# Kernel tuning notes

Hardware: AMD Instinct MI355X
Metric: run time of the kernel (lower is better)

The kernel has to match this reference:

```python
import jax, jax.numpy as jnp
import numpy as np
import math

H = 32          # num heads
D_NOPE = 128
D_ROPE = 64
D_QK = D_NOPE + D_ROPE   # 192
D_V = 128
KV_LORA = 512
EPS = 1e-6
ROPE_THETA = 10000.0
FACTOR = 40.0
BETA_FAST, BETA_SLOW = 32.0, 1.0
ORIG_MAX_POS = 4096
MSCALE_ALL_DIM = 1.0


def _yarn_inv_freq():
    dim = D_ROPE
    pos_freqs = ROPE_THETA ** (np.arange(0, dim, 2, dtype=np.float64) / dim)
    inv_extra = 1.0 / pos_freqs
    inv_inter = 1.0 / (FACTOR * pos_freqs)

    def corr_dim(n_rot):
        return dim * math.log(ORIG_MAX_POS / (n_rot * 2 * math.pi)) / (2 * math.log(ROPE_THETA))
    low = max(math.floor(corr_dim(BETA_FAST)), 0)
    high = min(math.ceil(corr_dim(BETA_SLOW)), dim - 1)
    ramp = np.clip((np.arange(dim // 2, dtype=np.float64) - low) / max(high - low, 1e-3), 0, 1)
    inv_freq_mask = 1.0 - ramp  # extrapolation_factor = 1
    inv_freq = inv_inter * (1 - inv_freq_mask) + inv_extra * inv_freq_mask
    return jnp.asarray(inv_freq, dtype=jnp.float32)  # [D_ROPE//2]


def _apply_rope_gptj(x, cos, sin):
    # x: [T, n, D_ROPE]; cos/sin: [T, D_ROPE//2]; interleaved (is_neox_style=False)
    x2 = x.reshape(*x.shape[:-1], D_ROPE // 2, 2)
    x1, xo = x2[..., 0], x2[..., 1]
    c = cos[:, None, :]
    s = sin[:, None, :]
    r1 = x1 * c - xo * s
    r2 = xo * c + x1 * s
    return jnp.stack([r1, r2], axis=-1).reshape(x.shape)


def _rmsnorm(x, w):
    var = jnp.mean(x.astype(jnp.float32) ** 2, axis=-1, keepdims=True)
    return (x * jax.lax.rsqrt(var + EPS)) * w


def setup_inputs() -> dict:
    key = jax.random.key(0)
    ks = jax.random.split(key, 8)
    T, HID = 2048, 4096
    def w(k, shape, fan_in):
        return jax.random.normal(k, shape, dtype=jnp.float32) * (1.0 / math.sqrt(fan_in))
    return {
        "positions": jnp.arange(T, dtype=jnp.int32),
        "hidden_states": jax.random.normal(ks[0], (T, HID), dtype=jnp.float32),
        "Wqa": w(ks[1], (HID, 1536), HID),
        "q_a_ln": jnp.ones((1536,), dtype=jnp.float32),
        "Wqb": w(ks[2], (1536, H * D_QK), 1536),
        "Wkva": w(ks[3], (HID, KV_LORA + D_ROPE), HID),
        "kv_a_ln": jnp.ones((KV_LORA,), dtype=jnp.float32),
        "Wkvb": w(ks[4], (KV_LORA, H * (D_NOPE + D_V)), KV_LORA),
        "Wo": w(ks[5], (H * D_V, HID), H * D_V),
    }


def reference(positions, hidden_states, Wqa, q_a_ln, Wqb, Wkva, kv_a_ln, Wkvb, Wo):
    T = hidden_states.shape[0]
    # softmax scaling with yarn mscale correction
    mscale = 0.1 * MSCALE_ALL_DIM * math.log(FACTOR) + 1.0
    scaling = (D_QK ** -0.5) * mscale * mscale

    # --- low-rank Q path ---
    q = hidden_states @ Wqa                       # [T, 1536]
    q = _rmsnorm(q, q_a_ln)
    q = (q @ Wqb).reshape(T, H, D_QK)             # [T, H, 192]
    q_nope, q_pe = q[..., :D_NOPE], q[..., D_NOPE:]

    # --- low-rank latent KV path ---
    latent = hidden_states @ Wkva                 # [T, 576]
    kv_a = _rmsnorm(latent[:, :KV_LORA], kv_a_ln) # [T, 512]
    k_pe = latent[:, None, KV_LORA:]              # [T, 1, 64]
    kv = (kv_a @ Wkvb).reshape(T, H, D_NOPE + D_V)
    k_nope = kv[..., :D_NOPE]                     # [T, H, 128]
    v = kv[..., D_NOPE:]                          # [T, H, 128]

    # --- decoupled RoPE on rope slice only ---
    inv_freq = _yarn_inv_freq()
    freqs = positions.astype(jnp.float32)[:, None] * inv_freq[None, :]  # [T, 32]
    cos, sin = jnp.cos(freqs), jnp.sin(freqs)
    q_pe = _apply_rope_gptj(q_pe, cos, sin)       # [T, H, 64]
    k_pe = _apply_rope_gptj(k_pe, cos, sin)       # [T, 1, 64]

    q = jnp.concatenate([q_nope, q_pe], axis=-1)                      # [T, H, 192]
    k = jnp.concatenate([k_nope, jnp.broadcast_to(k_pe, (T, H, D_ROPE))], axis=-1)

    # --- causal MHA over assembled K/V ---
    scores = jnp.einsum('thd,shd->hts', q, k) * scaling               # [H, T, T]
    causal = positions[None, :, None] >= positions[None, None, :]
    scores = jnp.where(causal, scores, jnp.finfo(scores.dtype).min)
    probs = jax.nn.softmax(scores, axis=-1)
    attn = jnp.einsum('hts,shd->thd', probs, v).reshape(T, H * D_V)
    return attn @ Wo                                                   # [T, 4096]
```

## Files before the change

kernel.cpp:

```cpp
#include <hip/hip_runtime.h>
#include <math.h>

typedef __bf16 bf16x8 __attribute__((ext_vector_type(8)));
typedef float f32x4 __attribute__((ext_vector_type(4)));
typedef unsigned short u16;
typedef unsigned int u32;

#define T_SEQ 2048
#define NHEAD 32

__device__ __forceinline__ u16 f2bu(float f){
  u32 u = __float_as_uint(f);
  u32 r = (u + 0x7fffu + ((u >> 16) & 1u)) >> 16;
  return (u16)r;
}

__device__ __forceinline__ void gload_lds16(const void* g, void* l){
  __builtin_amdgcn_global_load_lds((const __attribute__((address_space(1))) u32*)g,
                                   (__attribute__((address_space(3))) u32*)l, 16, 0, 0);
}

__global__ void cast_f32_bf16(const float* __restrict__ in, u16* __restrict__ out, int n4){
  int i = blockIdx.x * blockDim.x + threadIdx.x;
  int stride = gridDim.x * blockDim.x;
  for (; i < n4; i += stride){
    float4 v = ((const float4*)in)[i];
    ushort4 o;
    o.x = f2bu(v.x); o.y = f2bu(v.y); o.z = f2bu(v.z); o.w = f2bu(v.w);
    ((ushort4*)out)[i] = o;
  }
}

__global__ void transpose_cast(const float* __restrict__ src, u16* __restrict__ dst,
                               int K, int N){
  __shared__ float tile[64][65];
  int k0 = blockIdx.x * 64, n0 = blockIdx.y * 64;
  int lr = threadIdx.x >> 6, lc = threadIdx.x & 63;
  #pragma unroll
  for (int i = 0; i < 16; i++){
    int r = lr * 16 + i;
    int n = n0 + lc;
    float v = (n < N) ? src[(size_t)(k0 + r) * N + n] : 0.f;
    tile[r][lc] = v;
  }
  __syncthreads();
  #pragma unroll
  for (int i = 0; i < 16; i++){
    int nr = lr * 16 + i;
    dst[(size_t)(n0 + nr) * K + k0 + lc] = f2bu(tile[lc][nr]);
  }
}

__global__ void rope_table(const int* __restrict__ positions, float* __restrict__ cosT,
                           float* __restrict__ sinT, float lo, float denom){
  int idx = blockIdx.x * blockDim.x + threadIdx.x;
  if (idx >= T_SEQ * 32) return;
  int t = idx >> 5, i = idx & 31;
  float pf = powf(10000.f, (float)i / 32.f);
  float inv_extra = 1.f / pf;
  float inv_inter = 1.f / (40.f * pf);
  float ramp = fminf(fmaxf(((float)i - lo) / denom, 0.f), 1.f);
  float invf = inv_inter * ramp + inv_extra * (1.f - ramp);
  float fr = (float)positions[t] * invf;
  cosT[idx] = cosf(fr);
  sinT[idx] = sinf(fr);
}

__global__ void rmsnorm_cast(const float* __restrict__ in, int istride, int n,
                             const float* __restrict__ w, u16* __restrict__ out, int ostride){
  int row = blockIdx.x;
  const float* x = in + (size_t)row * istride;
  float ss = 0.f;
  for (int c = threadIdx.x; c < n; c += blockDim.x){ float v = x[c]; ss += v * v; }
  #pragma unroll
  for (int off = 1; off < 64; off <<= 1) ss += __shfl_xor(ss, off);
  __shared__ float wsum[4];
  if ((threadIdx.x & 63) == 0) wsum[threadIdx.x >> 6] = ss;
  __syncthreads();
  float tot = wsum[0] + wsum[1] + wsum[2] + wsum[3];
  float scale = rsqrtf(tot / (float)n + 1e-6f);
  for (int c = threadIdx.x; c < n; c += blockDim.x)
    out[(size_t)row * ostride + c] = f2bu(x[c] * scale * w[c]);
}

__global__ void rope_kpe(const float* __restrict__ lat, int lstride, int loff,
                         const float* __restrict__ cosT,
                         const float* __restrict__ sinT, u16* __restrict__ kpe){
  int idx = blockIdx.x * blockDim.x + threadIdx.x;
  if (idx >= T_SEQ * 32) return;
  int t = idx >> 5, i = idx & 31;
  float x1 = lat[(size_t)t * lstride + loff + 2 * i];
  float x2 = lat[(size_t)t * lstride + loff + 2 * i + 1];
  float c = cosT[idx], s = sinT[idx];
  kpe[t * 64 + 2 * i]     = f2bu(x1 * c - x2 * s);
  kpe[t * 64 + 2 * i + 1] = f2bu(x2 * c + x1 * s);
}

__global__ void kpe_bcast(const u16* __restrict__ kpe, u16* __restrict__ Kp){
  int idx = blockIdx.x * blockDim.x + threadIdx.x;
  if (idx >= NHEAD * T_SEQ * 16) return;
  int h = idx >> 15;
  int rem = idx & 32767;
  int t = rem >> 4, j = rem & 15;
  ushort4 v = ((const ushort4*)(kpe + t * 64))[j];
  ((ushort4*)(Kp + (size_t)h * T_SEQ * 192 + (size_t)t * 192 + 128))[j] = v;
}

__global__ void build_vt(const u16* __restrict__ Vtmp, u16* __restrict__ Vt){
  __shared__ u16 tile[128][72];
  int t0 = blockIdx.x * 64;
  int h = blockIdx.y;
  #pragma unroll
  for (int i = 0; i < 32; i++){
    int lin = threadIdx.x + i * 256;
    int tt = lin >> 7, dd = lin & 127;
    tile[dd][tt] = Vtmp[(size_t)(t0 + tt) * 4096 + h * 128 + dd];
  }
  __syncthreads();
  #pragma unroll
  for (int i = 0; i < 32; i++){
    int lin = threadIdx.x + i * 256;
    int dd = lin >> 6, tt = lin & 63;
    Vt[(size_t)(h * 128 + dd) * T_SEQ + t0 + tt] = tile[dd][tt];
  }
}

template<int EPI>
__global__ __launch_bounds__(256) void gemm_bt(const u16* __restrict__ A, const u16* __restrict__ BT,
                                               float* __restrict__ C, u16* __restrict__ O1,
                                               u16* __restrict__ O2,
                                               const float* __restrict__ cosT,
                                               const float* __restrict__ sinT,
                                               float scaling, int M, int N, int K){
  __shared__ __align__(1024) char lds[32768];
  const int tid = threadIdx.x;
  const int wave = tid >> 6, lane = tid & 63;
  const int lg = lane >> 4, lm = lane & 15;

  int gx = gridDim.x;
  int nwg = gx * gridDim.y;
  int orig = blockIdx.y * gx + blockIdx.x;
  int qq = nwg >> 3, rr = nwg & 7, xc = orig & 7, rest = orig >> 3;
  int wg = (xc < rr ? xc * (qq + 1) : rr * (qq + 1) + (xc - rr) * qq) + rest;
  const int bn = (wg % gx) * 128, bm = (wg / gx) * 128;

  const int wr = (wave >> 1) * 64, wc = (wave & 1) * 64;
  f32x4 acc[4][4] = {};
  int srow[2], scol[2], soff[2];
  #pragma unroll
  for (int j = 0; j < 2; j++){
    int o = (wave * 2 + j) * 1024 + lane * 16;
    int row = o >> 6;
    int cg = ((o >> 4) & 3) ^ ((row >> 1) & 3);
    srow[j] = row; scol[j] = cg * 8; soff[j] = (wave * 2 + j) * 1024;
  }

  #pragma unroll
  for (int j = 0; j < 2; j++){
    gload_lds16(A  + (size_t)(bm + srow[j]) * K + scol[j], lds + soff[j]);
    gload_lds16(BT + (size_t)(bn + srow[j]) * K + scol[j], lds + 16384 + soff[j]);
  }

  int cur = 0;
  for (int k0 = 0; k0 < K; k0 += 32){
    if (k0 + 32 < K){
      char* dA = lds + (cur ^ 1) * 8192;
      char* dB = lds + 16384 + (cur ^ 1) * 8192;
      #pragma unroll
      for (int j = 0; j < 2; j++){
        gload_lds16(A  + (size_t)(bm + srow[j]) * K + k0 + 32 + scol[j], dA + soff[j]);
        gload_lds16(BT + (size_t)(bn + srow[j]) * K + k0 + 32 + scol[j], dB + soff[j]);
      }
      asm volatile("s_waitcnt vmcnt(4)" ::: "memory");
    } else {
      asm volatile("s_waitcnt vmcnt(0)" ::: "memory");
    }
    __builtin_amdgcn_sched_barrier(0);
    __builtin_amdgcn_s_barrier();

    const char* ldsA = lds + cur * 8192;
    const char* ldsB = lds + 16384 + cur * 8192;
    bf16x8 af[4], bfr[4];
    #pragma unroll
    for (int m = 0; m < 4; m++){
      int r = wr + m * 16 + lm;
      af[m] = *(const bf16x8*)(ldsA + r * 64 + ((lg ^ ((r >> 1) & 3)) << 4));
    }
    #pragma unroll
    for (int n = 0; n < 4; n++){
      int r = wc + n * 16 + lm;
      bfr[n] = *(const bf16x8*)(ldsB + r * 64 + ((lg ^ ((r >> 1) & 3)) << 4));
    }
    __builtin_amdgcn_s_setprio(1);
    #pragma unroll
    for (int m = 0; m < 4; m++)
      #pragma unroll
      for (int n = 0; n < 4; n++)
        acc[m][n] = __builtin_amdgcn_mfma_f32_16x16x32_bf16(af[m], bfr[n], acc[m][n], 0, 0, 0);
    __builtin_amdgcn_s_setprio(0);
    __builtin_amdgcn_s_barrier();
    cur ^= 1;
  }

  #pragma unroll
  for (int m = 0; m < 4; m++)
    #pragma unroll
    for (int n = 0; n < 4; n++)
      #pragma unroll
      for (int q = 0; q < 4; q++){
        int r = bm + wr + m * 16 + lg * 4 + q;
        int c = bn + wc + n * 16 + lm;
        float v = acc[m][n][q];
        if (EPI == 0){
          C[(size_t)r * N + c] = v;
        } else if (EPI == 1){
          float vp = __shfl_xor(v, 1);
          int h = c / 192, d = c - h * 192;
          float outv;
          if (d < 128) outv = v;
          else {
            int i = (d - 128) >> 1;
            float co = cosT[r * 32 + i], si = sinT[r * 32 + i];
            outv = (d & 1) ? (v * co + vp * si) : (v * co - vp * si);
          }
          O1[(size_t)h * T_SEQ * 192 + (size_t)r * 192 + d] = f2bu(outv * scaling);
        } else {
          int h = c >> 8, d = c & 255;
          if (d < 128) O1[(size_t)h * T_SEQ * 192 + (size_t)r * 192 + d] = f2bu(v);
          else         O2[(size_t)r * 4096 + h * 128 + (d - 128)] = f2bu(v);
        }
      }
}

__global__ __launch_bounds__(512, 1) void flash_attn(const u16* __restrict__ Qp, const u16* __restrict__ Kp,
                                                     const u16* __restrict__ Vt, u16* __restrict__ attnb){
  const int b = blockIdx.x;
  const int h = (b & 7) + 8 * ((b >> 3) & 3);
  const int s = b >> 5;
  const int tid = threadIdx.x;
  const int wave = tid >> 6, lane = tid & 63;
  const int lg = lane >> 4, lm = lane & 15;

  __shared__ __align__(1024) char lds[100352];
  char* ldsK = lds;
  char* ldsV = lds + 49152;
  u16*  Pw   = (u16*)(lds + 81920 + wave * 2304);

  const u16* KpH = Kp + (size_t)h * T_SEQ * 192;
  const u16* VtH = Vt + (size_t)h * 128 * T_SEQ;

  int kO[3], kSrc[3];
  #pragma unroll
  for (int j = 0; j < 3; j++){
    int o = (tid + 512 * j) * 16;
    int r = o / 384, c = (o % 384) >> 4;
    kO[j] = o; kSrc[j] = r * 192 + ((c ^ (r & 7)) << 3);
  }
  int vO[2], vSrc[2];
  #pragma unroll
  for (int j = 0; j < 2; j++){
    int o = (tid + 512 * j) * 16;
    int d = o >> 7, c = (o & 127) >> 4;
    vO[j] = o; vSrc[j] = d * T_SEQ + ((c ^ (d & 7)) << 3);
  }

  #pragma unroll 1
  for (int rep = 0; rep < 2; rep++){
    const int qt = rep ? s : (15 - s);
    const int qbase = qt * 128 + wave * 16;
    const int nt = 2 * qt + 2;

    __syncthreads();

    bf16x8 qf[6];
    const u16* Qbase = Qp + (size_t)(h * T_SEQ + qbase + lm) * 192 + lg * 8;
    #pragma unroll
    for (int dk = 0; dk < 6; dk++) qf[dk] = *(const bf16x8*)(Qbase + dk * 32);

    f32x4 o_[8] = {};
    float m_[4], l_[4];
    #pragma unroll
    for (int q = 0; q < 4; q++){ m_[q] = -3.0e38f; l_[q] = 0.f; }

    #pragma unroll
    for (int j = 0; j < 3; j++) gload_lds16(KpH + kSrc[j], ldsK + kO[j]);
    #pragma unroll
    for (int j = 0; j < 2; j++) gload_lds16(VtH + vSrc[j], ldsV + vO[j]);

    for (int kt = 0; kt < nt; kt++){
      const int t0 = kt * 64;
      const int bsel = kt & 1;
      asm volatile("s_waitcnt vmcnt(0)" ::: "memory");
      __builtin_amdgcn_sched_barrier(0);
      __builtin_amdgcn_s_barrier();
      if (kt + 1 < nt){
        const int t1 = t0 + 64;
        char* Kd = ldsK + (bsel ^ 1) * 24576;
        char* Vd = ldsV + (bsel ^ 1) * 16384;
        #pragma unroll
        for (int j = 0; j < 3; j++) gload_lds16(KpH + (size_t)t1 * 192 + kSrc[j], Kd + kO[j]);
        #pragma unroll
        for (int j = 0; j < 2; j++) gload_lds16(VtH + vSrc[j] + t1, Vd + vO[j]);
      }
      const char* Kb = ldsK + bsel * 24576;
      const char* Vb = ldsV + bsel * 16384;

      f32x4 s_[4] = {};
      __builtin_amdgcn_s_setprio(1);
      #pragma unroll
      for (int hh = 0; hh < 4; hh++){
        const int r = hh * 16 + lm;
        const int rb = r * 384, rx = r & 7;
        #pragma unroll
        for (int dk = 0; dk < 6; dk++){
          bf16x8 kf = *(const bf16x8*)(Kb + rb + (((dk * 4 + lg) ^ rx) << 4));
          s_[hh] = __builtin_amdgcn_mfma_f32_16x16x32_bf16(qf[dk], kf, s_[hh], 0, 0, 0);
        }
      }
      __builtin_amdgcn_s_setprio(0);
      #pragma unroll
      for (int hh = 0; hh < 4; hh++)
        #pragma unroll
        for (int q = 0; q < 4; q++){
          int col = t0 + hh * 16 + lm;
          int qrow = qbase + lg * 4 + q;
          if (col > qrow) s_[hh][q] = -3.0e38f;
        }
      float pm[4];
      #pragma unroll
      for (int q = 0; q < 4; q++)
        pm[q] = fmaxf(fmaxf(s_[0][q], s_[1][q]), fmaxf(s_[2][q], s_[3][q]));
      int ok = (pm[0] <= m_[0] + 8.f) & (pm[1] <= m_[1] + 8.f) &
               (pm[2] <= m_[2] + 8.f) & (pm[3] <= m_[3] + 8.f);
      if (!__all(ok)){
        #pragma unroll
        for (int q = 0; q < 4; q++){
          float v = pm[q];
          #pragma unroll
          for (int off = 8; off; off >>= 1) v = fmaxf(v, __shfl_xor(v, off));
          float mn = fmaxf(m_[q], v);
          float alpha = (m_[q] <= -1.0e37f) ? 0.f : __expf(m_[q] - mn);
          l_[q] *= alpha;
          #pragma unroll
          for (int n = 0; n < 8; n++) o_[n][q] *= alpha;
          m_[q] = mn;
        }
      }
      #pragma unroll
      for (int q = 0; q < 4; q++){
        #pragma unroll
        for (int hh = 0; hh < 4; hh++){
          float p = __expf(s_[hh][q] - m_[q]);
          l_[q] += p;
          Pw[(lg * 4 + q) * 72 + hh * 16 + lm] = f2bu(p);
        }
      }
      asm volatile("s_waitcnt lgkmcnt(0)" ::: "memory");
      __builtin_amdgcn_sched_barrier(0);
      __builtin_amdgcn_s_setprio(1);
      #pragma unroll
      for (int ks = 0; ks < 2; ks++){
        bf16x8 pf = *(const bf16x8*)((const char*)Pw + lm * 144 + ks * 64 + lg * 16);
        #pragma unroll
        for (int n = 0; n < 8; n++){
          const int d = n * 16 + lm;
          bf16x8 vf = *(const bf16x8*)(Vb + d * 128 + (((ks * 4 + lg) ^ (d & 7)) << 4));
          o_[n] = __builtin_amdgcn_mfma_f32_16x16x32_bf16(pf, vf, o_[n], 0, 0, 0);
        }
      }
      __builtin_amdgcn_s_setprio(0);
    }

    #pragma unroll
    for (int q = 0; q < 4; q++){
      #pragma unroll
      for (int off = 8; off; off >>= 1) l_[q] += __shfl_xor(l_[q], off);
    }
    float inv[4];
    #pragma unroll
    for (int q = 0; q < 4; q++) inv[q] = 1.f / l_[q];
    #pragma unroll
    for (int n = 0; n < 8; n++)
      #pragma unroll
      for (int q = 0; q < 4; q++){
        int r = qbase + lg * 4 + q;
        attnb[(size_t)r * 4096 + h * 128 + n * 16 + lm] = f2bu(o_[n][q] * inv[q]);
      }
  }
}

extern "C" void kernel_launch(void* const* d_in, const int* in_sizes, int n_in,
                              void* d_out, int out_size, void* d_ws, size_t ws_size,
                              hipStream_t stream){
  const int*   positions = (const int*)d_in[0];
  const float* hidden    = (const float*)d_in[1];
  const float* Wqa       = (const float*)d_in[2];
  const float* q_a_ln    = (const float*)d_in[3];
  const float* Wqb       = (const float*)d_in[4];
  const float* Wkva      = (const float*)d_in[5];
  const float* kv_a_ln   = (const float*)d_in[6];
  const float* Wkvb      = (const float*)d_in[7];
  const float* Wo        = (const float*)d_in[8];
  float* out = (float*)d_out;
  char* ws = (char*)d_ws;

  const size_t o_hid  = 0;
  const size_t o_cos  = 16777216;
  const size_t o_sin  = 17039360;
  const size_t o_comb = 17301504;
  const size_t o_qln  = 35127296;
  const size_t o_kva  = 41418752;
  const size_t o_kpe  = 43515904;
  const size_t o_W    = 43778048;
  const size_t o_Qp   = 77332480;
  const size_t o_Kp   = 102498304;
  const size_t o_Vtmp = 127664128;
  const size_t o_Vt   = 144441344;
  const size_t o_att  = 161218560;

  u16*   hidB = (u16*)(ws + o_hid);
  float* cosT = (float*)(ws + o_cos);
  float* sinT = (float*)(ws + o_sin);
  float* comb = (float*)(ws + o_comb);
  u16*   qln  = (u16*)(ws + o_qln);
  u16*   kva  = (u16*)(ws + o_kva);
  u16*   kpe  = (u16*)(ws + o_kpe);
  u16*   Wt   = (u16*)(ws + o_W);
  u16*   Qp   = (u16*)(ws + o_Qp);
  u16*   Kp   = (u16*)(ws + o_Kp);
  u16*   Vtmp = (u16*)(ws + o_Vtmp);
  u16*   Vt   = (u16*)(ws + o_Vt);
  u16*   attnb= (u16*)(ws + o_att);

  double mscale = 0.1 * log(40.0) + 1.0;
  float scaling = (float)(pow(192.0, -0.5) * mscale * mscale);
  const double PI = 3.14159265358979323846;
  double cd_fast = 64.0 * log(4096.0 / (32.0 * 2.0 * PI)) / (2.0 * log(10000.0));
  double cd_slow = 64.0 * log(4096.0 / ( 1.0 * 2.0 * PI)) / (2.0 * log(10000.0));
  double lo_d = fmax(floor(cd_fast), 0.0);
  double hi_d = fmin(ceil(cd_slow), 63.0);
  float lo = (float)lo_d;
  float denom = (float)fmax(hi_d - lo_d, 0.001);

  cast_f32_bf16<<<2048, 256, 0, stream>>>(hidden, hidB, T_SEQ * 4096 / 4);
  rope_table<<<256, 256, 0, stream>>>(positions, cosT, sinT, lo, denom);
  transpose_cast<<<dim3(4096 / 64, 1536 / 64), 256, 0, stream>>>(Wqa, Wt, 4096, 1536);
  transpose_cast<<<dim3(4096 / 64, 640 / 64), 256, 0, stream>>>(Wkva, Wt + (size_t)1536 * 4096, 4096, 576);
  gemm_bt<0><<<dim3(2176 / 128, 2048 / 128), 256, 0, stream>>>(hidB, Wt, comb, nullptr, nullptr,
                                                               nullptr, nullptr, 0.f, 2048, 2176, 4096);
  rmsnorm_cast<<<2048, 256, 0, stream>>>(comb, 2176, 1536, q_a_ln, qln, 1536);
  rmsnorm_cast<<<2048, 256, 0, stream>>>(comb + 1536, 2176, 512, kv_a_ln, kva, 512);
  rope_kpe<<<256, 256, 0, stream>>>(comb, 2176, 2048, cosT, sinT, kpe);
  transpose_cast<<<dim3(1536 / 64, 6144 / 64), 256, 0, stream>>>(Wqb, Wt, 1536, 6144);
  gemm_bt<1><<<dim3(6144 / 128, 2048 / 128), 256, 0, stream>>>(qln, Wt, nullptr, Qp, nullptr,
                                                               cosT, sinT, scaling, 2048, 6144, 1536);
  transpose_cast<<<dim3(512 / 64, 8192 / 64), 256, 0, stream>>>(Wkvb, Wt, 512, 8192);
  gemm_bt<2><<<dim3(8192 / 128, 2048 / 128), 256, 0, stream>>>(kva, Wt, nullptr, Kp, Vtmp,
                                                               nullptr, nullptr, 0.f, 2048, 8192, 512);
  kpe_bcast<<<NHEAD * T_SEQ * 16 / 256, 256, 0, stream>>>(kpe, Kp);
  build_vt<<<dim3(T_SEQ / 64, NHEAD), 256, 0, stream>>>(Vtmp, Vt);
  flash_attn<<<256, 512, 0, stream>>>(Qp, Kp, Vt, attnb);
  transpose_cast<<<dim3(4096 / 64, 4096 / 64), 256, 0, stream>>>(Wo, Wt, 4096, 4096);
  gemm_bt<0><<<dim3(4096 / 128, 2048 / 128), 256, 0, stream>>>(attnb, Wt, out, nullptr, nullptr,
                                                               nullptr, nullptr, 0.f, 2048, 4096, 4096);
}
```

Baseline: 441.8 us.

## Drop k_pe broadcast, triple-buffer K/V in attention, vectorize weight transpose

Three separate changes. Kp now holds only the 128-wide nope part per head, and flash_attn gathers the shared rope slice straight from the single kpe buffer, so the kpe_bcast kernel and its per-head copies go away. The attention K/V staging moves from double to triple buffering with a partial vmcnt wait, so loads run two tiles ahead, at the cost of more LDS per block. transpose_cast now reads float4 and writes ushort4 to cut the number of memory transactions.

```diff
diff --git a/kernel.cpp b/kernel.cpp
--- a/kernel.cpp
+++ b/kernel.cpp
@@ -35,19 +35,30 @@
                                int K, int N){
   __shared__ float tile[64][65];
   int k0 = blockIdx.x * 64, n0 = blockIdx.y * 64;
-  int lr = threadIdx.x >> 6, lc = threadIdx.x & 63;
-  #pragma unroll
-  for (int i = 0; i < 16; i++){
-    int r = lr * 16 + i;
-    int n = n0 + lc;
-    float v = (n < N) ? src[(size_t)(k0 + r) * N + n] : 0.f;
-    tile[r][lc] = v;
+  int t = threadIdx.x;
+  int rr = t >> 4, c4 = (t & 15) * 4;
+  #pragma unroll
+  for (int i = 0; i < 4; i++){
+    int r = rr + i * 16;
+    int n = n0 + c4;
+    float4 v;
+    if (n < N) v = *(const float4*)(src + (size_t)(k0 + r) * N + n);
+    else       v = make_float4(0.f, 0.f, 0.f, 0.f);
+    tile[r][c4]     = v.x;
+    tile[r][c4 + 1] = v.y;
+    tile[r][c4 + 2] = v.z;
+    tile[r][c4 + 3] = v.w;
   }
   __syncthreads();
   #pragma unroll
-  for (int i = 0; i < 16; i++){
-    int nr = lr * 16 + i;
-    dst[(size_t)(n0 + nr) * K + k0 + lc] = f2bu(tile[lc][nr]);
+  for (int i = 0; i < 4; i++){
+    int n = rr + i * 16;
+    ushort4 o;
+    o.x = f2bu(tile[c4 + 0][n]);
+    o.y = f2bu(tile[c4 + 1][n]);
+    o.z = f2bu(tile[c4 + 2][n]);
+    o.w = f2bu(tile[c4 + 3][n]);
+    *(ushort4*)(dst + (size_t)(n0 + n) * K + k0 + c4) = o;
   }
 }
 
@@ -96,16 +107,6 @@
   kpe[t * 64 + 2 * i + 1] = f2bu(x2 * c + x1 * s);
 }
 
-__global__ void kpe_bcast(const u16* __restrict__ kpe, u16* __restrict__ Kp){
-  int idx = blockIdx.x * blockDim.x + threadIdx.x;
-  if (idx >= NHEAD * T_SEQ * 16) return;
-  int h = idx >> 15;
-  int rem = idx & 32767;
-  int t = rem >> 4, j = rem & 15;
-  ushort4 v = ((const ushort4*)(kpe + t * 64))[j];
-  ((ushort4*)(Kp + (size_t)h * T_SEQ * 192 + (size_t)t * 192 + 128))[j] = v;
-}
-
 __global__ void build_vt(const u16* __restrict__ Vtmp, u16* __restrict__ Vt){
   __shared__ u16 tile[128][72];
   int t0 = blockIdx.x * 64;
@@ -140,8 +141,8 @@
   int gx = gridDim.x;
   int nwg = gx * gridDim.y;
   int orig = blockIdx.y * gx + blockIdx.x;
-  int qq = nwg >> 3, rr = nwg & 7, xc = orig & 7, rest = orig >> 3;
-  int wg = (xc < rr ? xc * (qq + 1) : rr * (qq + 1) + (xc - rr) * qq) + rest;
+  int qq = nwg >> 3, rr_ = nwg & 7, xc = orig & 7, rest = orig >> 3;
+  int wg = (xc < rr_ ? xc * (qq + 1) : rr_ * (qq + 1) + (xc - rr_) * qq) + rest;
   const int bn = (wg % gx) * 128, bm = (wg / gx) * 128;
 
   const int wr = (wave >> 1) * 64, wc = (wave & 1) * 64;
@@ -226,14 +227,15 @@
           O1[(size_t)h * T_SEQ * 192 + (size_t)r * 192 + d] = f2bu(outv * scaling);
         } else {
           int h = c >> 8, d = c & 255;
-          if (d < 128) O1[(size_t)h * T_SEQ * 192 + (size_t)r * 192 + d] = f2bu(v);
+          if (d < 128) O1[(size_t)h * T_SEQ * 128 + (size_t)r * 128 + d] = f2bu(v);
           else         O2[(size_t)r * 4096 + h * 128 + (d - 128)] = f2bu(v);
         }
       }
 }
 
 __global__ __launch_bounds__(512, 1) void flash_attn(const u16* __restrict__ Qp, const u16* __restrict__ Kp,
-                                                     const u16* __restrict__ Vt, u16* __restrict__ attnb){
+                                                     const u16* __restrict__ kpe, const u16* __restrict__ Vt,
+                                                     u16* __restrict__ attnb){
   const int b = blockIdx.x;
   const int h = (b & 7) + 8 * ((b >> 3) & 3);
   const int s = b >> 5;
@@ -241,20 +243,21 @@
   const int wave = tid >> 6, lane = tid & 63;
   const int lg = lane >> 4, lm = lane & 15;
 
-  __shared__ __align__(1024) char lds[100352];
-  char* ldsK = lds;
-  char* ldsV = lds + 49152;
-  u16*  Pw   = (u16*)(lds + 81920 + wave * 2304);
-
-  const u16* KpH = Kp + (size_t)h * T_SEQ * 192;
+  __shared__ __align__(1024) char lds[141312];
+  u16* Pw = (u16*)(lds + 122880 + wave * 2304);
+
+  const u16* KpH = Kp + (size_t)h * T_SEQ * 128;
   const u16* VtH = Vt + (size_t)h * 128 * T_SEQ;
 
-  int kO[3], kSrc[3];
+  int kO[3], kLoc[3], kPE[3];
   #pragma unroll
   for (int j = 0; j < 3; j++){
-    int o = (tid + 512 * j) * 16;
-    int r = o / 384, c = (o % 384) >> 4;
-    kO[j] = o; kSrc[j] = r * 192 + ((c ^ (r & 7)) << 3);
+    int o = tid + 512 * j;
+    int r = o / 24, c = o - r * 24;
+    int cx = c ^ (r & 7);
+    kO[j] = o * 16;
+    if (cx < 16){ kPE[j] = 0; kLoc[j] = r * 128 + cx * 8; }
+    else        { kPE[j] = 1; kLoc[j] = r * 64 + (cx - 16) * 8; }
   }
   int vO[2], vSrc[2];
   #pragma unroll
@@ -263,6 +266,20 @@
     int d = o >> 7, c = (o & 127) >> 4;
     vO[j] = o; vSrc[j] = d * T_SEQ + ((c ^ (d & 7)) << 3);
   }
+
+  #define STAGE_KV(t, bi)                                                              \
+    do {                                                                               \
+      char* _k = lds + (bi) * 24576;                                                   \
+      char* _v = lds + 73728 + (bi) * 16384;                                           \
+      _Pragma("unroll")                                                                \
+      for (int j = 0; j < 3; j++){                                                     \
+        const u16* _s = kPE[j] ? (kpe + (size_t)(t) * 4096 + kLoc[j])                  \
+                               : (KpH + (size_t)(t) * 8192 + kLoc[j]);                 \
+        gload_lds16(_s, _k + kO[j]);                                                   \
+      }                                                                                \
+      _Pragma("unroll")                                                                \
+      for (int j = 0; j < 2; j++) gload_lds16(VtH + vSrc[j] + (t) * 64, _v + vO[j]);   \
+    } while (0)
 
   #pragma unroll 1
   for (int rep = 0; rep < 2; rep++){
@@ -282,28 +299,23 @@
     #pragma unroll
     for (int q = 0; q < 4; q++){ m_[q] = -3.0e38f; l_[q] = 0.f; }
 
-    #pragma unroll
-    for (int j = 0; j < 3; j++) gload_lds16(KpH + kSrc[j], ldsK + kO[j]);
-    #pragma unroll
-    for (int j = 0; j < 2; j++) gload_lds16(VtH + vSrc[j], ldsV + vO[j]);
-
+    STAGE_KV(0, 0);
+    if (nt > 1) STAGE_KV(1, 1);
+
+    int cur = 0;
+    #pragma unroll 1
     for (int kt = 0; kt < nt; kt++){
       const int t0 = kt * 64;
-      const int bsel = kt & 1;
-      asm volatile("s_waitcnt vmcnt(0)" ::: "memory");
+      if (kt < nt - 1) asm volatile("s_waitcnt vmcnt(5)" ::: "memory");
+      else             asm volatile("s_waitcnt vmcnt(0)" ::: "memory");
       __builtin_amdgcn_sched_barrier(0);
       __builtin_amdgcn_s_barrier();
-      if (kt + 1 < nt){
-        const int t1 = t0 + 64;
-        char* Kd = ldsK + (bsel ^ 1) * 24576;
-        char* Vd = ldsV + (bsel ^ 1) * 16384;
-        #pragma unroll
-        for (int j = 0; j < 3; j++) gload_lds16(KpH + (size_t)t1 * 192 + kSrc[j], Kd + kO[j]);
-        #pragma unroll
-        for (int j = 0; j < 2; j++) gload_lds16(VtH + vSrc[j] + t1, Vd + vO[j]);
-      }
-      const char* Kb = ldsK + bsel * 24576;
-      const char* Vb = ldsV + bsel * 16384;
+      if (kt + 2 < nt){
+        int nb = cur + 2; if (nb >= 3) nb -= 3;
+        STAGE_KV(kt + 2, nb);
+      }
+      const char* Kb = lds + cur * 24576;
+      const char* Vb = lds + 73728 + cur * 16384;
 
       f32x4 s_[4] = {};
       __builtin_amdgcn_s_setprio(1);
@@ -369,6 +381,7 @@
         }
       }
       __builtin_amdgcn_s_setprio(0);
+      cur = (cur == 2) ? 0 : cur + 1;
     }
 
     #pragma unroll
@@ -387,6 +400,7 @@
         attnb[(size_t)r * 4096 + h * 128 + n * 16 + lm] = f2bu(o_[n][q] * inv[q]);
       }
   }
+  #undef STAGE_KV
 }
 
 extern "C" void kernel_launch(void* const* d_in, const int* in_sizes, int n_in,
@@ -407,24 +421,24 @@
   const size_t o_hid  = 0;
   const size_t o_cos  = 16777216;
   const size_t o_sin  = 17039360;
-  const size_t o_comb = 17301504;
-  const size_t o_qln  = 35127296;
-  const size_t o_kva  = 41418752;
-  const size_t o_kpe  = 43515904;
+  const size_t o_kpe  = 17301504;
+  const size_t o_comb = 17563648;
+  const size_t o_qln  = 35389440;
+  const size_t o_kva  = 41680896;
   const size_t o_W    = 43778048;
   const size_t o_Qp   = 77332480;
   const size_t o_Kp   = 102498304;
-  const size_t o_Vtmp = 127664128;
-  const size_t o_Vt   = 144441344;
-  const size_t o_att  = 161218560;
+  const size_t o_Vtmp = 119275520;
+  const size_t o_Vt   = 136052736;
+  const size_t o_att  = 152829952;
 
   u16*   hidB = (u16*)(ws + o_hid);
   float* cosT = (float*)(ws + o_cos);
   float* sinT = (float*)(ws + o_sin);
+  u16*   kpe  = (u16*)(ws + o_kpe);
   float* comb = (float*)(ws + o_comb);
   u16*   qln  = (u16*)(ws + o_qln);
   u16*   kva  = (u16*)(ws + o_kva);
-  u16*   kpe  = (u16*)(ws + o_kpe);
   u16*   Wt   = (u16*)(ws + o_W);
   u16*   Qp   = (u16*)(ws + o_Qp);
   u16*   Kp   = (u16*)(ws + o_Kp);
@@ -457,9 +471,8 @@
   transpose_cast<<<dim3(512 / 64, 8192 / 64), 256, 0, stream>>>(Wkvb, Wt, 512, 8192);
   gemm_bt<2><<<dim3(8192 / 128, 2048 / 128), 256, 0, stream>>>(kva, Wt, nullptr, Kp, Vtmp,
                                                                nullptr, nullptr, 0.f, 2048, 8192, 512);
-  kpe_bcast<<<NHEAD * T_SEQ * 16 / 256, 256, 0, stream>>>(kpe, Kp);
   build_vt<<<dim3(T_SEQ / 64, NHEAD), 256, 0, stream>>>(Vtmp, Vt);
-  flash_attn<<<256, 512, 0, stream>>>(Qp, Kp, Vt, attnb);
+  flash_attn<<<256, 512, 0, stream>>>(Qp, Kp, kpe, Vt, attnb);
   transpose_cast<<<dim3(4096 / 64, 4096 / 64), 256, 0, stream>>>(Wo, Wt, 4096, 4096);
   gemm_bt<0><<<dim3(4096 / 128, 2048 / 128), 256, 0, stream>>>(attnb, Wt, out, nullptr, nullptr,
                                                                nullptr, nullptr, 0.f, 2048, 4096, 4096);
```

Measured after the change: 412.6 us. -6.6%, faster.
